# Kernel optimization log

Measured on AMD Instinct MI355X. Metric: run time of the kernel, lower is better.

## Reference

```python
import jax, jax.numpy as jnp
import numpy as np

NUM_SCALES = 3      # num_scales
SPARSITY = 5        # base_sparsity (neighbors per scale)
DT = 0.1
HALF_DT = DT / 2.0
CG_ITERS = 20       # cg_max_iter
CG_TOL = 1e-6       # cg_tol


def ham_matvec(v, w):
    """Multi-scale sparse (stencil) Hamiltonian matvec along last dim.
    H = sum_{m,j} w[m,j] * (2 I - shift(+off) - shift(-off)), off = 2^m * (j+1).
    Real symmetric -> Cayley step is unitary."""
    out = jnp.zeros_like(v)
    for m in range(NUM_SCALES):
        for j in range(SPARSITY):
            off = (2 ** m) * (j + 1)
            out = out + w[m, j] * (2.0 * v - jnp.roll(v, off, axis=-1) - jnp.roll(v, -off, axis=-1))
    return out


def a_minus(x, w):
    """(I + i*dt/2*H) in real-block form. x: [B,S,D,2]."""
    vr, vi = x[..., 0], x[..., 1]
    Hvr = ham_matvec(vr, w)
    Hvi = ham_matvec(vi, w)
    return jnp.stack([vr - HALF_DT * Hvi, vi + HALF_DT * Hvr], axis=-1)


def _dot(a, b):
    # per-(B,S) system inner product over (D, 2)
    return jnp.sum(a * b, axis=(-2, -1))


def cg_solve(w, b):
    """Batched CG solve a_minus(x) = b with x0 = 0, fixed iteration count with
    per-system convergence masking (frozen once residual < tol * ||b||)."""
    x = jnp.zeros_like(b)
    r = b              # b - A(0)
    p = r
    rs = _dot(r, r)    # [B, S]
    thresh = (CG_TOL ** 2) * jnp.maximum(rs, 1e-30)

    def body(carry, _):
        x, r, p, rs = carry
        active = rs > thresh
        Ap = a_minus(p, w)
        alpha = jnp.where(active, rs / (_dot(p, Ap) + 1e-30), 0.0)
        x = x + alpha[..., None, None] * p
        r = r - alpha[..., None, None] * Ap
        rs_new = _dot(r, r)
        beta = jnp.where(active, rs_new / (rs + 1e-30), 0.0)
        p = jnp.where(active[..., None, None], r + beta[..., None, None] * p, p)
        rs = jnp.where(active, rs_new, rs)
        return (x, r, p, rs), None

    (x, _, _, _), _ = jax.lax.scan(body, (x, r, p, rs), None, length=CG_ITERS)
    return x


def setup_inputs() -> dict:
    key = jax.random.key(0)
    k1, k2, k3 = jax.random.split(key, 3)
    B, S, D = 8, 2048, 1024
    psi_r = jax.random.normal(k1, (B, S, D), dtype=jnp.float32)
    psi_i = jax.random.normal(k2, (B, S, D), dtype=jnp.float32)
    alpha = 0.1 * jnp.ones((D,), dtype=jnp.float32)               # nonlinear_alpha init
    ham_w = 0.1 * jax.random.uniform(k3, (NUM_SCALES, SPARSITY), dtype=jnp.float32) + 0.01
    return {"psi_r": psi_r, "psi_i": psi_i, "alpha": alpha, "ham_w": ham_w}


def reference(psi_r, psi_i, alpha, ham_w):
    # nonlinear phase rotation: exp(i * alpha * |psi|^2 / mean|psi|^2)
    intensity = psi_r * psi_r + psi_i * psi_i
    intensity = intensity / (jnp.mean(intensity, axis=-1, keepdims=True) + 1e-8)
    phase = alpha * intensity
    c, s = jnp.cos(phase), jnp.sin(phase)
    rot_r = psi_r * c - psi_i * s
    rot_i = psi_r * s + psi_i * c
    # rhs = (I - i*dt/2*H) psi_rot  (real-block form)
    Hr = ham_matvec(rot_r, ham_w)
    Hi = ham_matvec(rot_i, ham_w)
    rhs = jnp.stack([rot_r + HALF_DT * Hi, rot_i - HALF_DT * Hr], axis=-1)  # [B,S,D,2]
    # Cayley: psi_out = (I + i*dt/2*H)^{-1} rhs via CG
    return cg_solve(ham_w, rhs)
```

## Files before the change

### kernel.cpp

```cpp
#include <hip/hip_runtime.h>
#include <utility>

typedef float v2f __attribute__((ext_vector_type(2)));

#define HDT 0.05f
#define KSTEPS 5

__device__ __forceinline__ float bf2f(unsigned int u) {
    return __uint_as_float(u << 16);
}
__device__ __forceinline__ unsigned int f2bf(float x) {
    unsigned int b = __float_as_uint(x);
    return (b + 0x7FFFu + ((b >> 16) & 1u)) >> 16;
}
__device__ __forceinline__ float rfl(float x) {
    return __int_as_float(__builtin_amdgcn_readfirstlane(__float_as_int(x)));
}

template <int... Is, class F>
__device__ __forceinline__ void static_for_impl(std::integer_sequence<int, Is...>, F&& f) {
    (f(std::integral_constant<int, Is>{}), ...);
}
template <int N, class F>
__device__ __forceinline__ void static_for(F&& f) {
    static_for_impl(std::make_integer_sequence<int, N>{}, (F&&)f);
}

__host__ __device__ constexpr int cidx(int d) {
    int a = d < 0 ? -d : d;
    return (a==0)?0:(a==1)?1:(a==2)?2:(a==3)?3:(a==4)?4:(a==5)?5:(a==6)?6:
           (a==8)?7:(a==10)?8:(a==12)?9:(a==16)?10:(a==20)?11:-1;
}

__global__ void detect_dtype(const unsigned int* __restrict__ w, int* __restrict__ flag) {
    int cnt = 0;
    for (int i = threadIdx.x; i < 4096; i += 64) {
        unsigned int e = (w[i] >> 7) & 0xFFu;
        cnt += (e >= 0x78u && e <= 0x82u) ? 1 : 0;
    }
    #pragma unroll
    for (int off = 32; off; off >>= 1) cnt += __shfl_xor(cnt, off, 64);
    if (threadIdx.x == 0) *flag = (cnt > 2048) ? 1 : 0;
}

__global__ __launch_bounds__(256, 3)
void cayley_main(const void* __restrict__ psi_r, const void* __restrict__ psi_i,
                 const void* __restrict__ alpha, const void* __restrict__ ham_w,
                 void* __restrict__ out, const int* __restrict__ flagp)
{
    __shared__ float4 lds4[2048];

    const int lane = threadIdx.x & 63;
    const int wv   = threadIdx.x >> 6;
    const int sys  = (blockIdx.x << 2) + wv;
    const int sysq = wv << 9;

    const bool isbf = (*flagp) != 0;

    float hw[15];
    if (isbf) {
        const unsigned short* p = (const unsigned short*)ham_w;
        #pragma unroll
        for (int i = 0; i < 15; ++i) hw[i] = bf2f((unsigned int)p[i]);
    } else {
        const float* p = (const float*)ham_w;
        #pragma unroll
        for (int i = 0; i < 15; ++i) hw[i] = p[i];
    }
    float cs[12];
    {
        float s = 0.f;
        #pragma unroll
        for (int i = 0; i < 15; ++i) s += hw[i];
        cs[0]  = rfl( 2.f*HDT*s);
        cs[1]  = rfl(-HDT* hw[0]);
        cs[2]  = rfl(-HDT*(hw[1]+hw[5]));
        cs[3]  = rfl(-HDT* hw[2]);
        cs[4]  = rfl(-HDT*(hw[3]+hw[6]+hw[10]));
        cs[5]  = rfl(-HDT* hw[4]);
        cs[6]  = rfl(-HDT* hw[7]);
        cs[7]  = rfl(-HDT*(hw[8]+hw[11]));
        cs[8]  = rfl(-HDT* hw[9]);
        cs[9]  = rfl(-HDT* hw[12]);
        cs[10] = rfl(-HDT* hw[13]);
        cs[11] = rfl(-HDT* hw[14]);
    }

    int raddr[28];
    #pragma unroll
    for (int g = 0; g < 28; ++g) {
        int qd = (8*lane - 10 + g) & 511;
        raddr[g] = sysq + (qd ^ ((qd >> 3) & 7));
    }
    int waddr[8];
    #pragma unroll
    for (int k = 0; k < 8; ++k) {
        int qd = 8*lane + k;
        waddr[k] = sysq + (qd ^ ((qd >> 3) & 7));
    }

    float pr[16], pq[16], al[16];
    if (isbf) {
        const unsigned short* bR = (const unsigned short*)psi_r + (size_t)sys*1024 + lane*16;
        const unsigned short* bI = (const unsigned short*)psi_i + (size_t)sys*1024 + lane*16;
        const unsigned short* bA = (const unsigned short*)alpha  + lane*16;
        static_for<2>([&](auto hI) {
            constexpr int h = hI.value;
            uint4 a = ((const uint4*)bR)[h];
            uint4 b = ((const uint4*)bI)[h];
            uint4 c = ((const uint4*)bA)[h];
            pr[h*8+0]=bf2f(a.x&0xFFFFu); pr[h*8+1]=bf2f(a.x>>16);
            pr[h*8+2]=bf2f(a.y&0xFFFFu); pr[h*8+3]=bf2f(a.y>>16);
            pr[h*8+4]=bf2f(a.z&0xFFFFu); pr[h*8+5]=bf2f(a.z>>16);
            pr[h*8+6]=bf2f(a.w&0xFFFFu); pr[h*8+7]=bf2f(a.w>>16);
            pq[h*8+0]=bf2f(b.x&0xFFFFu); pq[h*8+1]=bf2f(b.x>>16);
            pq[h*8+2]=bf2f(b.y&0xFFFFu); pq[h*8+3]=bf2f(b.y>>16);
            pq[h*8+4]=bf2f(b.z&0xFFFFu); pq[h*8+5]=bf2f(b.z>>16);
            pq[h*8+6]=bf2f(b.w&0xFFFFu); pq[h*8+7]=bf2f(b.w>>16);
            al[h*8+0]=bf2f(c.x&0xFFFFu); al[h*8+1]=bf2f(c.x>>16);
            al[h*8+2]=bf2f(c.y&0xFFFFu); al[h*8+3]=bf2f(c.y>>16);
            al[h*8+4]=bf2f(c.z&0xFFFFu); al[h*8+5]=bf2f(c.z>>16);
            al[h*8+6]=bf2f(c.w&0xFFFFu); al[h*8+7]=bf2f(c.w>>16);
        });
    } else {
        const float* fR = (const float*)psi_r + (size_t)sys*1024 + lane*16;
        const float* fI = (const float*)psi_i + (size_t)sys*1024 + lane*16;
        const float* fA = (const float*)alpha  + lane*16;
        static_for<4>([&](auto hI) {
            constexpr int h = hI.value;
            float4 a = ((const float4*)fR)[h];
            float4 b = ((const float4*)fI)[h];
            float4 c = ((const float4*)fA)[h];
            pr[4*h]=a.x; pr[4*h+1]=a.y; pr[4*h+2]=a.z; pr[4*h+3]=a.w;
            pq[4*h]=b.x; pq[4*h+1]=b.y; pq[4*h+2]=b.z; pq[4*h+3]=b.w;
            al[4*h]=c.x; al[4*h+1]=c.y; al[4*h+2]=c.z; al[4*h+3]=c.w;
        });
    }

    float ssum = 0.f;
    #pragma unroll
    for (int k = 0; k < 16; ++k) ssum += pr[k]*pr[k] + pq[k]*pq[k];
    #pragma unroll
    for (int off = 32; off; off >>= 1) ssum += __shfl_xor(ssum, off, 64);
    const float inv = 1.f / (ssum * (1.f/1024.f) + 1e-8f);

    v2f cur[16];
    static_for<16>([&](auto kI) {
        constexpr int k = kI.value;
        float inten = (pr[k]*pr[k] + pq[k]*pq[k]) * inv;
        float ph = al[k] * inten;
        float cc = __cosf(ph), sn = __sinf(ph);
        cur[k].x = pr[k]*cc - pq[k]*sn;
        cur[k].y = pr[k]*sn + pq[k]*cc;
    });

    v2f acc[16], b[16], t[16];

    auto ldswrite = [&](v2f (&arr)[16]) {
        static_for<8>([&](auto kI) {
            constexpr int k8 = kI.value;
            lds4[waddr[k8]] = make_float4(arr[2*k8].x, arr[2*k8].y,
                                          arr[2*k8+1].x, arr[2*k8+1].y);
        });
    };
    auto stencil = [&]() {
        static_for<16>([&](auto kI) { acc[kI.value].x = 0.f; acc[kI.value].y = 0.f; });
        static_for<28>([&](auto gI) {
            constexpr int g = gI.value;
            float4 q = lds4[raddr[g]];
            v2f e0; e0.x = q.x; e0.y = q.y;
            v2f e1; e1.x = q.z; e1.y = q.w;
            static_for<16>([&](auto kI) {
                constexpr int k = kI.value;
                constexpr int id0 = cidx(2*g     - 20 - k);
                constexpr int id1 = cidx(2*g + 1 - 20 - k);
                if constexpr (id0 >= 0) acc[k] += cs[id0] * e0;
                if constexpr (id1 >= 0) acc[k] += cs[id1] * e1;
            });
        });
    };

    ldswrite(cur);
    stencil();
    static_for<16>([&](auto kI) {
        constexpr int k = kI.value;
        b[k].x = cur[k].x + acc[k].y;
        b[k].y = cur[k].y - acc[k].x;
    });
    ldswrite(b);

    #pragma unroll 1
    for (int itn = 0; itn < KSTEPS; ++itn) {
        stencil();
        static_for<16>([&](auto kI) {
            constexpr int k = kI.value;
            t[k].x = b[k].x + acc[k].y;
            t[k].y = b[k].y - acc[k].x;
        });
        if (itn != KSTEPS - 1) ldswrite(t);
    }

    if (isbf) {
        unsigned short* po = (unsigned short*)out + (size_t)sys*2048 + lane*32;
        uint4* po4 = (uint4*)po;
        static_for<4>([&](auto hI) {
            constexpr int h = hI.value;
            uint4 v;
            v.x = f2bf(t[4*h+0].x) | (f2bf(t[4*h+0].y) << 16);
            v.y = f2bf(t[4*h+1].x) | (f2bf(t[4*h+1].y) << 16);
            v.z = f2bf(t[4*h+2].x) | (f2bf(t[4*h+2].y) << 16);
            v.w = f2bf(t[4*h+3].x) | (f2bf(t[4*h+3].y) << 16);
            po4[h] = v;
        });
    } else {
        float* po = (float*)out + (size_t)sys*2048 + lane*32;
        static_for<8>([&](auto kI) {
            constexpr int k8 = kI.value;
            *(float4*)(po + 4*k8) = make_float4(t[2*k8].x, t[2*k8].y,
                                                t[2*k8+1].x, t[2*k8+1].y);
        });
    }
}

extern "C" void kernel_launch(void* const* d_in, const int* in_sizes, int n_in,
                              void* d_out, int out_size, void* d_ws, size_t ws_size,
                              hipStream_t stream)
{
    (void)in_sizes; (void)n_in; (void)out_size; (void)ws_size;
    detect_dtype<<<dim3(1), dim3(64), 0, stream>>>((const unsigned int*)d_in[0], (int*)d_ws);
    cayley_main<<<dim3(4096), dim3(256), 0, stream>>>(d_in[0], d_in[1], d_in[2], d_in[3],
                                                      d_out, (const int*)d_ws);
}
```

Baseline: 305.7 us.

## Use one-wave blocks, in-kernel dtype detection, and register reuse in stencil

The separate dtype-detection kernel is removed; each wave now detects the dtype itself with a ballot over the first 64 words of psi_r. Blocks shrink to a single 64-thread wave with a 512-entry LDS buffer, and the grid grows to 16384. The stencil takes the lane's own 16 elements straight from registers instead of reloading them from LDS, so LDS reads per stencil drop from 28 to 20. The intent is to cut a kernel launch and some LDS traffic. The cost is one redundant global read per wave and possibly different occupancy and scheduling with single-wave blocks.

```diff
diff --git a/kernel.cpp b/kernel.cpp
--- a/kernel.cpp
+++ b/kernel.cpp
@@ -32,30 +32,22 @@
            (a==8)?7:(a==10)?8:(a==12)?9:(a==16)?10:(a==20)?11:-1;
 }
 
-__global__ void detect_dtype(const unsigned int* __restrict__ w, int* __restrict__ flag) {
-    int cnt = 0;
-    for (int i = threadIdx.x; i < 4096; i += 64) {
-        unsigned int e = (w[i] >> 7) & 0xFFu;
-        cnt += (e >= 0x78u && e <= 0x82u) ? 1 : 0;
-    }
-    #pragma unroll
-    for (int off = 32; off; off >>= 1) cnt += __shfl_xor(cnt, off, 64);
-    if (threadIdx.x == 0) *flag = (cnt > 2048) ? 1 : 0;
-}
-
-__global__ __launch_bounds__(256, 3)
+__global__ __launch_bounds__(64, 4)
 void cayley_main(const void* __restrict__ psi_r, const void* __restrict__ psi_i,
                  const void* __restrict__ alpha, const void* __restrict__ ham_w,
-                 void* __restrict__ out, const int* __restrict__ flagp)
+                 void* __restrict__ out)
 {
-    __shared__ float4 lds4[2048];
-
-    const int lane = threadIdx.x & 63;
-    const int wv   = threadIdx.x >> 6;
-    const int sys  = (blockIdx.x << 2) + wv;
-    const int sysq = wv << 9;
-
-    const bool isbf = (*flagp) != 0;
+    __shared__ float4 lds4[512];
+
+    const int lane = threadIdx.x;
+    const int sys  = blockIdx.x;
+
+    {
+    }
+    unsigned int w0 = ((const unsigned int*)psi_r)[lane];
+    unsigned int ex = (w0 >> 7) & 0xFFu;
+    unsigned long long bm = __ballot(ex >= 0x78u && ex <= 0x82u);
+    const bool isbf = __builtin_popcountll(bm) > 32;
 
     float hw[15];
     if (isbf) {
@@ -86,17 +78,18 @@
         cs[11] = rfl(-HDT* hw[14]);
     }
 
-    int raddr[28];
-    #pragma unroll
-    for (int g = 0; g < 28; ++g) {
+    int raddr[20];
+    #pragma unroll
+    for (int ri = 0; ri < 20; ++ri) {
+        int g = (ri < 10) ? ri : (ri + 8);
         int qd = (8*lane - 10 + g) & 511;
-        raddr[g] = sysq + (qd ^ ((qd >> 3) & 7));
+        raddr[ri] = qd ^ ((qd >> 3) & 7);
     }
     int waddr[8];
     #pragma unroll
     for (int k = 0; k < 8; ++k) {
         int qd = 8*lane + k;
-        waddr[k] = sysq + (qd ^ ((qd >> 3) & 7));
+        waddr[k] = qd ^ ((qd >> 3) & 7);
     }
 
     float pr[16], pq[16], al[16];
@@ -163,13 +156,20 @@
                                           arr[2*k8+1].x, arr[2*k8+1].y);
         });
     };
-    auto stencil = [&]() {
+    auto stencil = [&](const v2f (&src)[16]) {
         static_for<16>([&](auto kI) { acc[kI.value].x = 0.f; acc[kI.value].y = 0.f; });
         static_for<28>([&](auto gI) {
             constexpr int g = gI.value;
-            float4 q = lds4[raddr[g]];
-            v2f e0; e0.x = q.x; e0.y = q.y;
-            v2f e1; e1.x = q.z; e1.y = q.w;
+            v2f e0, e1;
+            if constexpr (g >= 10 && g <= 17) {
+                e0 = src[2*(g-10)];
+                e1 = src[2*(g-10)+1];
+            } else {
+                constexpr int ri = (g < 10) ? g : (g - 8);
+                float4 q = lds4[raddr[ri]];
+                e0.x = q.x; e0.y = q.y;
+                e1.x = q.z; e1.y = q.w;
+            }
             static_for<16>([&](auto kI) {
                 constexpr int k = kI.value;
                 constexpr int id0 = cidx(2*g     - 20 - k);
@@ -181,17 +181,18 @@
     };
 
     ldswrite(cur);
-    stencil();
+    stencil(cur);
     static_for<16>([&](auto kI) {
         constexpr int k = kI.value;
         b[k].x = cur[k].x + acc[k].y;
         b[k].y = cur[k].y - acc[k].x;
     });
     ldswrite(b);
+    static_for<16>([&](auto kI) { t[kI.value] = b[kI.value]; });
 
     #pragma unroll 1
     for (int itn = 0; itn < KSTEPS; ++itn) {
-        stencil();
+        stencil(t);
         static_for<16>([&](auto kI) {
             constexpr int k = kI.value;
             t[k].x = b[k].x + acc[k].y;
@@ -226,8 +227,7 @@
                               void* d_out, int out_size, void* d_ws, size_t ws_size,
                               hipStream_t stream)
 {
-    (void)in_sizes; (void)n_in; (void)out_size; (void)ws_size;
-    detect_dtype<<<dim3(1), dim3(64), 0, stream>>>((const unsigned int*)d_in[0], (int*)d_ws);
-    cayley_main<<<dim3(4096), dim3(256), 0, stream>>>(d_in[0], d_in[1], d_in[2], d_in[3],
-                                                      d_out, (const int*)d_ws);
-}
+    (void)in_sizes; (void)n_in; (void)out_size; (void)d_ws; (void)ws_size;
+    cayley_main<<<dim3(16384), dim3(64), 0, stream>>>(d_in[0], d_in[1], d_in[2], d_in[3],
+                                                      d_out);
+}
```

Result: slower. 421.6 us (+37.9%).
